# Kernel tuning notes

Measured on AMD Instinct MI355X. Metric: run time of the kernel, lower is better.

The kernel has to match this reference:

```python
import jax, jax.numpy as jnp
import numpy as np

N_RAYS, N_SAMPLES = 65536, 128


def setup_inputs() -> dict:
    key = jax.random.key(0)
    k1, k2, k3, k4, k5 = jax.random.split(key, 5)
    return {
        "sigma_vals": jax.random.normal(k1, (N_RAYS, N_SAMPLES), dtype=jnp.float32),
        "rgb_vals": jax.random.uniform(k2, (N_RAYS, N_SAMPLES, 3), dtype=jnp.float32),
        "dists": jax.random.uniform(k3, (N_RAYS, N_SAMPLES), dtype=jnp.float32),
        "z_vals": jax.random.uniform(k4, (N_RAYS, N_SAMPLES), dtype=jnp.float32),
        "bg_color": jax.random.uniform(k5, (N_RAYS, 3), dtype=jnp.float32),
    }


def composite(sigma_vals, dists):
    # tau = relu(sigma) * dist; alpha = 1 - exp(-tau)
    tau = jax.nn.relu(sigma_vals) * dists
    alpha = 1.0 - jnp.exp(-tau)                       # [N, S]
    # inclusive cumprod of (1 - alpha + eps), with leading ones -> transmittance [N, S+1]
    trans = jnp.cumprod(1.0 - alpha + 1e-10, axis=-1)
    transmittance = jnp.concatenate(
        [jnp.ones_like(alpha[..., :1]), trans], axis=-1
    )
    w = alpha * transmittance[..., :-1]               # [N, S]
    return w, transmittance


def reference(sigma_vals, rgb_vals, dists, z_vals, bg_color):
    # Python-side compositing path of Raymarcher.render_train (thresh=0).
    weights, transmittance = composite(sigma_vals, dists)
    no_hit = transmittance[..., -1]                                    # [N]
    color = (weights[..., None] * rgb_vals).sum(axis=-2)               # [N, 3]
    color = color + no_hit[..., None] * bg_color                       # bg compositing
    depth = (weights * z_vals).sum(axis=-1)                            # [N]
    # pack color+depth into one array so the output is a single tensor [N, 4]
    return jnp.concatenate([color, depth[:, None]], axis=-1)
```

## Files before the change

kernel.cpp:

```cpp
#include <hip/hip_runtime.h>


#define SAMPLES 128

__global__ __launch_bounds__(256) void raymarch_composite(
    const float* __restrict__ sigma,
    const float* __restrict__ rgb,
    const float* __restrict__ dists,
    const float* __restrict__ zvals,
    const float* __restrict__ bg,
    float* __restrict__ out,
    int n_rays)
{
    const int lane = threadIdx.x & 63;
    const int wave = threadIdx.x >> 6;
    const int ray  = blockIdx.x * (blockDim.x >> 6) + wave;
    if (ray >= n_rays) return;

    const size_t base = (size_t)ray * SAMPLES;

    const float2 sg = *reinterpret_cast<const float2*>(sigma + base + 2 * lane);
    const float2 dt = *reinterpret_cast<const float2*>(dists + base + 2 * lane);
    const float2 zv = *reinterpret_cast<const float2*>(zvals + base + 2 * lane);

    const float* rgbp = rgb + base * 3 + 6 * lane;
    const float2 c01 = *reinterpret_cast<const float2*>(rgbp + 0);
    const float2 c23 = *reinterpret_cast<const float2*>(rgbp + 2);
    const float2 c45 = *reinterpret_cast<const float2*>(rgbp + 4);

    const float eps = 1e-10f;
    const float tau0 = fmaxf(sg.x, 0.0f) * dt.x;
    const float tau1 = fmaxf(sg.y, 0.0f) * dt.y;
    const float alpha0 = 1.0f - expf(-tau0);
    const float alpha1 = 1.0f - expf(-tau1);
    const float f0 = 1.0f - alpha0 + eps;
    const float f1 = 1.0f - alpha1 + eps;

    float scan = f0 * f1;
    #pragma unroll
    for (int off = 1; off < 64; off <<= 1) {
        const float up = __shfl_up(scan, off);
        scan *= (lane >= off) ? up : 1.0f;
    }
    float excl = __shfl_up(scan, 1);
    if (lane == 0) excl = 1.0f;
    const float no_hit = __shfl(scan, 63);

    const float w0 = alpha0 * excl;
    const float w1 = alpha1 * (excl * f0);

    float r = w0 * c01.x + w1 * c23.y;
    float g = w0 * c01.y + w1 * c45.x;
    float b = w0 * c23.x + w1 * c45.y;
    float d = w0 * zv.x  + w1 * zv.y;

    #pragma unroll
    for (int off = 32; off >= 1; off >>= 1) {
        r += __shfl_xor(r, off);
        g += __shfl_xor(g, off);
        b += __shfl_xor(b, off);
        d += __shfl_xor(d, off);
    }

    if (lane == 0) {
        const float bgr = bg[ray * 3 + 0];
        const float bgg = bg[ray * 3 + 1];
        const float bgb = bg[ray * 3 + 2];
        float4 o;
        o.x = r + no_hit * bgr;
        o.y = g + no_hit * bgg;
        o.z = b + no_hit * bgb;
        o.w = d;
        *reinterpret_cast<float4*>(out + (size_t)ray * 4) = o;
    }
}

extern "C" void kernel_launch(void* const* d_in, const int* in_sizes, int n_in,
                              void* d_out, int out_size, void* d_ws, size_t ws_size,
                              hipStream_t stream) {
    const float* sigma = (const float*)d_in[0];
    const float* rgb   = (const float*)d_in[1];
    const float* dists = (const float*)d_in[2];
    const float* zvals = (const float*)d_in[3];
    const float* bg    = (const float*)d_in[4];
    float* out = (float*)d_out;

    const int n_rays = in_sizes[0] / SAMPLES;
    const int waves_per_block = 256 / 64;
    const int grid = (n_rays + waves_per_block - 1) / waves_per_block;

    raymarch_composite<<<grid, 256, 0, stream>>>(sigma, rgb, dists, zvals, bg,
                                                 out, n_rays);
}
```

Measured before the change: 213.0 us.

## Process multiple rays per wave with software-prefetched loads and packed reduction

Each wave now handles eight rays in sequence and issues the next ray's loads before computing the current one, so memory latency overlaps with the scan and reduction. The four-channel butterfly reduction is rewritten as a transpose-style packed reduction: two xor-shuffle steps fold the four channels into one value per lane, followed by a single-value reduction, which cuts the shuffle count. The background fetch and output store are spread across lanes 0-3, the lane-63 broadcast uses readlane, and exp uses the fast intrinsic. The grid shrinks eightfold, which may lower the number of waves available to hide latency, and launch bounds now request higher occupancy.

```diff
diff --git a/kernel.cpp b/kernel.cpp
--- a/kernel.cpp
+++ b/kernel.cpp
@@ -2,39 +2,42 @@
 
 
 #define SAMPLES 128
+#define RAYS_PER_WAVE 8
 
-__global__ __launch_bounds__(256) void raymarch_composite(
-    const float* __restrict__ sigma,
-    const float* __restrict__ rgb,
-    const float* __restrict__ dists,
-    const float* __restrict__ zvals,
-    const float* __restrict__ bg,
-    float* __restrict__ out,
-    int n_rays)
+struct RayData {
+    float2 sg, dt, zv;
+    float2 c01, c23, c45;
+    float  bgv;
+};
+
+__device__ __forceinline__ RayData load_ray(
+    const float* __restrict__ sigma, const float* __restrict__ rgb,
+    const float* __restrict__ dists, const float* __restrict__ zvals,
+    const float* __restrict__ bg, int ray, int lane)
 {
-    const int lane = threadIdx.x & 63;
-    const int wave = threadIdx.x >> 6;
-    const int ray  = blockIdx.x * (blockDim.x >> 6) + wave;
-    if (ray >= n_rays) return;
+    RayData rd;
+    const size_t base = (size_t)ray * SAMPLES;
+    rd.sg = *reinterpret_cast<const float2*>(sigma + base + 2 * lane);
+    rd.dt = *reinterpret_cast<const float2*>(dists + base + 2 * lane);
+    rd.zv = *reinterpret_cast<const float2*>(zvals + base + 2 * lane);
+    const float* rgbp = rgb + base * 3 + 6 * lane;
+    rd.c01 = *reinterpret_cast<const float2*>(rgbp + 0);
+    rd.c23 = *reinterpret_cast<const float2*>(rgbp + 2);
+    rd.c45 = *reinterpret_cast<const float2*>(rgbp + 4);
+    rd.bgv = (lane < 3) ? bg[(size_t)ray * 3 + lane] : 0.0f;
+    return rd;
+}
 
-    const size_t base = (size_t)ray * SAMPLES;
-
-    const float2 sg = *reinterpret_cast<const float2*>(sigma + base + 2 * lane);
-    const float2 dt = *reinterpret_cast<const float2*>(dists + base + 2 * lane);
-    const float2 zv = *reinterpret_cast<const float2*>(zvals + base + 2 * lane);
-
-    const float* rgbp = rgb + base * 3 + 6 * lane;
-    const float2 c01 = *reinterpret_cast<const float2*>(rgbp + 0);
-    const float2 c23 = *reinterpret_cast<const float2*>(rgbp + 2);
-    const float2 c45 = *reinterpret_cast<const float2*>(rgbp + 4);
-
+__device__ __forceinline__ void process_ray(
+    const RayData& rd, int ray, int lane, float* __restrict__ out)
+{
     const float eps = 1e-10f;
-    const float tau0 = fmaxf(sg.x, 0.0f) * dt.x;
-    const float tau1 = fmaxf(sg.y, 0.0f) * dt.y;
-    const float alpha0 = 1.0f - expf(-tau0);
-    const float alpha1 = 1.0f - expf(-tau1);
-    const float f0 = 1.0f - alpha0 + eps;
-    const float f1 = 1.0f - alpha1 + eps;
+    const float tau0 = fmaxf(rd.sg.x, 0.0f) * rd.dt.x;
+    const float tau1 = fmaxf(rd.sg.y, 0.0f) * rd.dt.y;
+    const float a0 = 1.0f - __expf(-tau0);
+    const float a1 = 1.0f - __expf(-tau1);
+    const float f0 = 1.0f - a0 + eps;
+    const float f1 = 1.0f - a1 + eps;
 
     float scan = f0 * f1;
     #pragma unroll
@@ -44,34 +47,51 @@
     }
     float excl = __shfl_up(scan, 1);
     if (lane == 0) excl = 1.0f;
-    const float no_hit = __shfl(scan, 63);
+    const float no_hit =
+        __uint_as_float(__builtin_amdgcn_readlane(__float_as_uint(scan), 63));
 
-    const float w0 = alpha0 * excl;
-    const float w1 = alpha1 * (excl * f0);
+    const float w0 = a0 * excl;
+    const float w1 = a1 * (excl * f0);
 
-    float r = w0 * c01.x + w1 * c23.y;
-    float g = w0 * c01.y + w1 * c45.x;
-    float b = w0 * c23.x + w1 * c45.y;
-    float d = w0 * zv.x  + w1 * zv.y;
+    float r = w0 * rd.c01.x + w1 * rd.c23.y;
+    float g = w0 * rd.c01.y + w1 * rd.c45.x;
+    float b = w0 * rd.c23.x + w1 * rd.c45.y;
+    float d = w0 * rd.zv.x  + w1 * rd.zv.y;
 
+    const bool o1 = lane & 1;
+    const float X = (o1 ? g : r) + __shfl_xor(o1 ? r : g, 1);
+    const float Y = (o1 ? d : b) + __shfl_xor(o1 ? b : d, 1);
+    const bool o2 = lane & 2;
+    float Z = (o2 ? Y : X) + __shfl_xor(o2 ? X : Y, 2);
     #pragma unroll
-    for (int off = 32; off >= 1; off >>= 1) {
-        r += __shfl_xor(r, off);
-        g += __shfl_xor(g, off);
-        b += __shfl_xor(b, off);
-        d += __shfl_xor(d, off);
-    }
+    for (int off = 4; off < 64; off <<= 1) Z += __shfl_xor(Z, off);
 
-    if (lane == 0) {
-        const float bgr = bg[ray * 3 + 0];
-        const float bgg = bg[ray * 3 + 1];
-        const float bgb = bg[ray * 3 + 2];
-        float4 o;
-        o.x = r + no_hit * bgr;
-        o.y = g + no_hit * bgg;
-        o.z = b + no_hit * bgb;
-        o.w = d;
-        *reinterpret_cast<float4*>(out + (size_t)ray * 4) = o;
+    const float val = fmaf(no_hit, rd.bgv, Z);
+    if (lane < 4) out[(size_t)ray * 4 + lane] = val;
+}
+
+__global__ __launch_bounds__(256, 8) void raymarch_composite(
+    const float* __restrict__ sigma, const float* __restrict__ rgb,
+    const float* __restrict__ dists, const float* __restrict__ zvals,
+    const float* __restrict__ bg, float* __restrict__ out, int n_rays)
+{
+    const int lane  = threadIdx.x & 63;
+    const int wave  = threadIdx.x >> 6;
+    const int gwave = blockIdx.x * (blockDim.x >> 6) + wave;
+    const int ray0  = gwave * RAYS_PER_WAVE;
+    if (ray0 >= n_rays) return;
+
+    RayData cur = load_ray(sigma, rgb, dists, zvals, bg, ray0, lane);
+    #pragma unroll 1
+    for (int i = 0; i < RAYS_PER_WAVE; ++i) {
+        const int ray = ray0 + i;
+        if (ray >= n_rays) break;
+        RayData nxt;
+        const int nray = ray + 1;
+        if (i + 1 < RAYS_PER_WAVE && nray < n_rays)
+            nxt = load_ray(sigma, rgb, dists, zvals, bg, nray, lane);
+        process_ray(cur, ray, lane, out);
+        cur = nxt;
     }
 }
 
@@ -86,8 +106,9 @@
     float* out = (float*)d_out;
 
     const int n_rays = in_sizes[0] / SAMPLES;
+    const int n_waves = (n_rays + RAYS_PER_WAVE - 1) / RAYS_PER_WAVE;
     const int waves_per_block = 256 / 64;
-    const int grid = (n_rays + waves_per_block - 1) / waves_per_block;
+    const int grid = (n_waves + waves_per_block - 1) / waves_per_block;
 
     raymarch_composite<<<grid, 256, 0, stream>>>(sigma, rgb, dists, zvals, bg,
                                                  out, n_rays);
```

Result: slower. 227.0 us (+6.6%).

## Process four rays per wave with 16 lanes each and DPP scans

Applied to the files above, without the earlier changes.

Each wave now handles four rays, with 16 lanes per ray. Each lane loads 8 samples as float4 vectors and computes a local serial transmittance product and weighted sums. The cross-lane prefix product and the reductions use DPP row operations instead of full-wave shuffles, and the four output channels are written by four lanes. The aim is fewer shuffle instructions, wider memory loads and fewer blocks for this memory-bound kernel. In exchange, per-lane register use rises and the reduction logic becomes more intricate.

```diff
diff --git a/kernel.cpp b/kernel.cpp
--- a/kernel.cpp
+++ b/kernel.cpp
@@ -2,6 +2,14 @@
 
 
 #define SAMPLES 128
+#define LANES_PER_RAY 16
+
+template <int CTRL>
+__device__ __forceinline__ float fdpp(float oldv, float src) {
+    return __uint_as_float((unsigned)__builtin_amdgcn_update_dpp(
+        (int)__float_as_uint(oldv), (int)__float_as_uint(src),
+        CTRL, 0xF, 0xF, false));
+}
 
 __global__ __launch_bounds__(256) void raymarch_composite(
     const float* __restrict__ sigma,
@@ -13,65 +21,74 @@
     int n_rays)
 {
     const int lane = threadIdx.x & 63;
-    const int wave = threadIdx.x >> 6;
-    const int ray  = blockIdx.x * (blockDim.x >> 6) + wave;
+    const int gw   = blockIdx.x * (blockDim.x >> 6) + (threadIdx.x >> 6);
+    const int grp  = lane >> 4;
+    const int pos  = lane & 15;
+    const int ray  = gw * 4 + grp;
     if (ray >= n_rays) return;
 
-    const size_t base = (size_t)ray * SAMPLES;
+    const size_t sbase = (size_t)ray * SAMPLES + pos * 8;
+    const float4* sp = reinterpret_cast<const float4*>(sigma + sbase);
+    const float4* dp = reinterpret_cast<const float4*>(dists + sbase);
+    const float4* zp = reinterpret_cast<const float4*>(zvals + sbase);
+    const float4* cp = reinterpret_cast<const float4*>(
+        rgb + (size_t)ray * (SAMPLES * 3) + pos * 24);
 
-    const float2 sg = *reinterpret_cast<const float2*>(sigma + base + 2 * lane);
-    const float2 dt = *reinterpret_cast<const float2*>(dists + base + 2 * lane);
-    const float2 zv = *reinterpret_cast<const float2*>(zvals + base + 2 * lane);
+    const float4 s0 = sp[0], s1 = sp[1];
+    const float4 d0 = dp[0], d1 = dp[1];
+    const float4 z0 = zp[0], z1 = zp[1];
+    const float4 c0 = cp[0], c1 = cp[1], c2 = cp[2];
+    const float4 c3 = cp[3], c4 = cp[4], c5 = cp[5];
+    const float bgv = (pos < 3) ? bg[(size_t)ray * 3 + pos] : 0.0f;
 
-    const float* rgbp = rgb + base * 3 + 6 * lane;
-    const float2 c01 = *reinterpret_cast<const float2*>(rgbp + 0);
-    const float2 c23 = *reinterpret_cast<const float2*>(rgbp + 2);
-    const float2 c45 = *reinterpret_cast<const float2*>(rgbp + 4);
+    const float s[8] = {s0.x, s0.y, s0.z, s0.w, s1.x, s1.y, s1.z, s1.w};
+    const float d[8] = {d0.x, d0.y, d0.z, d0.w, d1.x, d1.y, d1.z, d1.w};
+    const float z[8] = {z0.x, z0.y, z0.z, z0.w, z1.x, z1.y, z1.z, z1.w};
+    const float c[24] = {c0.x, c0.y, c0.z, c0.w, c1.x, c1.y, c1.z, c1.w,
+                         c2.x, c2.y, c2.z, c2.w, c3.x, c3.y, c3.z, c3.w,
+                         c4.x, c4.y, c4.z, c4.w, c5.x, c5.y, c5.z, c5.w};
 
     const float eps = 1e-10f;
-    const float tau0 = fmaxf(sg.x, 0.0f) * dt.x;
-    const float tau1 = fmaxf(sg.y, 0.0f) * dt.y;
-    const float alpha0 = 1.0f - expf(-tau0);
-    const float alpha1 = 1.0f - expf(-tau1);
-    const float f0 = 1.0f - alpha0 + eps;
-    const float f1 = 1.0f - alpha1 + eps;
-
-    float scan = f0 * f1;
+    float t = 1.0f;
+    float r = 0.f, g = 0.f, b = 0.f, dep = 0.f;
     #pragma unroll
-    for (int off = 1; off < 64; off <<= 1) {
-        const float up = __shfl_up(scan, off);
-        scan *= (lane >= off) ? up : 1.0f;
-    }
-    float excl = __shfl_up(scan, 1);
-    if (lane == 0) excl = 1.0f;
-    const float no_hit = __shfl(scan, 63);
-
-    const float w0 = alpha0 * excl;
-    const float w1 = alpha1 * (excl * f0);
-
-    float r = w0 * c01.x + w1 * c23.y;
-    float g = w0 * c01.y + w1 * c45.x;
-    float b = w0 * c23.x + w1 * c45.y;
-    float d = w0 * zv.x  + w1 * zv.y;
-
-    #pragma unroll
-    for (int off = 32; off >= 1; off >>= 1) {
-        r += __shfl_xor(r, off);
-        g += __shfl_xor(g, off);
-        b += __shfl_xor(b, off);
-        d += __shfl_xor(d, off);
+    for (int i = 0; i < 8; ++i) {
+        const float tau = fmaxf(s[i], 0.0f) * d[i];
+        const float e   = __expf(-tau);
+        const float a   = 1.0f - e;
+        const float f   = e + eps;
+        const float w   = a * t;
+        r   = fmaf(w, c[3 * i + 0], r);
+        g   = fmaf(w, c[3 * i + 1], g);
+        b   = fmaf(w, c[3 * i + 2], b);
+        dep = fmaf(w, z[i], dep);
+        t *= f;
     }
 
-    if (lane == 0) {
-        const float bgr = bg[ray * 3 + 0];
-        const float bgg = bg[ray * 3 + 1];
-        const float bgb = bg[ray * 3 + 2];
-        float4 o;
-        o.x = r + no_hit * bgr;
-        o.y = g + no_hit * bgg;
-        o.z = b + no_hit * bgb;
-        o.w = d;
-        *reinterpret_cast<float4*>(out + (size_t)ray * 4) = o;
+    float sc = t;
+    sc *= fdpp<0x111>(1.0f, sc);
+    sc *= fdpp<0x112>(1.0f, sc);
+    sc *= fdpp<0x114>(1.0f, sc);
+    sc *= fdpp<0x118>(1.0f, sc);
+    const float excl = fdpp<0x111>(1.0f, sc);
+
+    const float no_hit = __shfl(sc, lane | 15);
+
+    r *= excl; g *= excl; b *= excl; dep *= excl;
+
+    const bool o1 = pos & 1;
+    float X  = o1 ? g : r, Xo = o1 ? r : g;
+    float Y  = o1 ? dep : b, Yo = o1 ? b : dep;
+    X += fdpp<0xB1>(0.0f, Xo);
+    Y += fdpp<0xB1>(0.0f, Yo);
+    const bool o2 = pos & 2;
+    float Z  = o2 ? Y : X, Zo = o2 ? X : Y;
+    Z += fdpp<0x4E>(0.0f, Zo);
+    Z += fdpp<0x124>(0.0f, Z);
+    Z += fdpp<0x128>(0.0f, Z);
+
+    if (pos < 4) {
+        out[(size_t)ray * 4 + pos] = fmaf(no_hit, bgv, Z);
     }
 }
 
@@ -86,8 +103,8 @@
     float* out = (float*)d_out;
 
     const int n_rays = in_sizes[0] / SAMPLES;
-    const int waves_per_block = 256 / 64;
-    const int grid = (n_rays + waves_per_block - 1) / waves_per_block;
+    const int rays_per_block = 16;
+    const int grid = (n_rays + rays_per_block - 1) / rays_per_block;
 
     raymarch_composite<<<grid, 256, 0, stream>>>(sigma, rgb, dists, zvals, bg,
                                                  out, n_rays);
```

Measured after the change: 217.0 us. About the same (+1.9%).
